# Kernel tuning notes

Hardware: AMD Instinct MI355X
Metric: run time of the kernel (lower is better)

Reference implementation:

```python
import jax, jax.numpy as jnp
import numpy as np

S, B, D, H, DH = 1024, 4, 1024, 16, 64


def setup_inputs() -> dict:
    key = jax.random.key(0)
    ks = jax.random.split(key, 12)
    inp = {
        "query": jax.random.normal(ks[0], (S, B, D), dtype=jnp.float32),
        "key": jax.random.normal(ks[1], (S, B, D), dtype=jnp.float32),
        "value": jax.random.normal(ks[2], (S, B, D), dtype=jnp.float32),
        "key_mask": jax.random.randint(ks[3], (S, B), 0, 2, dtype=jnp.int32),
        # per-head stacked projection weights (original loops nn.Linear per head)
        "Wq": jax.random.normal(ks[4], (H, D, DH), dtype=jnp.float32) * 0.02,
        "bq": jnp.zeros((H, DH), dtype=jnp.float32),
        "Wk": jax.random.normal(ks[5], (H, D, DH), dtype=jnp.float32) * 0.02,
        "bk": jnp.zeros((H, DH), dtype=jnp.float32),
        "Wv": jax.random.normal(ks[6], (H, D, DH), dtype=jnp.float32) * 0.02,
        "bv": jnp.zeros((H, DH), dtype=jnp.float32),
        "Wo": jax.random.normal(ks[7], (H * DH, D), dtype=jnp.float32) * 0.02,
        "bo": jnp.zeros((D,), dtype=jnp.float32),
    }
    return inp


def reference(query, key, value, key_mask, Wq, bq, Wk, bk, Wv, bv, Wo, bo):
    # query/key/value: [S, B, D] (seq-major, matching torch einsum 'imk,jmk->imj')
    q = jnp.einsum('smd,hdk->smhk', query, Wq) + bq  # [Sq, B, H, DH]
    k = jnp.einsum('smd,hdk->smhk', key, Wk) + bk    # [Sk, B, H, DH]
    v = jnp.einsum('smd,hdk->smhk', value, Wv) + bv  # [Sk, B, H, DH]

    scale = 1.0 / jnp.sqrt(jnp.float32(DH))
    scores = jnp.einsum('imhk,jmhk->himj', q, k) * scale  # [H, Sq, B, Sk]
    # key_mask: [Sk, B] -> transpose -> [B, Sk]; additive -1e18 masking
    scores = scores - key_mask.astype(jnp.float32).T * 1e18
    attn = jax.nn.softmax(scores, axis=-1)
    out = jnp.einsum('himj,jmhk->imhk', attn, v)  # [Sq, B, H, DH]
    concat = out.reshape(out.shape[0], out.shape[1], H * DH)
    return concat @ Wo + bo  # [Sq, B, D]
```

## Files before the change

kernel.cpp:

```cpp
#include <hip/hip_runtime.h>
#include <hip/hip_bf16.h>


typedef __attribute__((ext_vector_type(8))) short short8;
typedef __attribute__((ext_vector_type(4))) short short4_;
typedef __attribute__((ext_vector_type(4))) float f32x4;
typedef __attribute__((ext_vector_type(16))) float f32x16;
typedef __attribute__((ext_vector_type(8))) __bf16 bf16x8;
typedef __attribute__((ext_vector_type(4))) __bf16 bf16x4;

union B8 {
    short8 s;
    bf16x8 b;
    unsigned short u[8];
};
union B4 {
    short4_ s;
    bf16x4 b;
    unsigned short u[4];
    int i[2];
};

#if __has_builtin(__builtin_amdgcn_exp2f)
#define EXP2(x) __builtin_amdgcn_exp2f(x)
#else
#define EXP2(x) exp2f(x)
#endif
#if __has_builtin(__builtin_amdgcn_rcpf)
#define RCP(x) __builtin_amdgcn_rcpf(x)
#else
#define RCP(x) (1.0f / (x))
#endif

static __device__ __forceinline__ unsigned short f2bf_rne(float f) {
    union { float f; unsigned u; } v; v.f = f;
    unsigned r = v.u + 0x7FFFu + ((v.u >> 16) & 1u);
    return (unsigned short)(r >> 16);
}

static __device__ __forceinline__ void async_lds16(const void* g, const void* l) {
    __builtin_amdgcn_global_load_lds(
        (const __attribute__((address_space(1))) unsigned int*)(unsigned long long)g,
        (__attribute__((address_space(3))) unsigned int*)(unsigned int)(unsigned long long)l,
        16, 0, 0);
}

__global__ __launch_bounds__(256) void prep(
    const float* __restrict__ Wq, const float* __restrict__ Wk,
    const float* __restrict__ Wv, const float* __restrict__ Wo,
    const float* __restrict__ query, const float* __restrict__ key,
    const float* __restrict__ value,
    unsigned short* __restrict__ WT,
    unsigned short* __restrict__ qA, unsigned short* __restrict__ kA,
    unsigned short* __restrict__ vA) {
    const int t = threadIdx.x;
    const int z = blockIdx.z;

    if (z >= 4) {
        const int zz = z - 4;
        const int tensor = zz >> 2;
        const int part = zz & 3;
        const float* src = (tensor == 0) ? query : (tensor == 1) ? key : value;
        unsigned short* dst = (tensor == 0) ? qA : (tensor == 1) ? kA : vA;
        const int blk = blockIdx.y * 16 + blockIdx.x;
        const size_t base = (size_t)part * 1048576 + (size_t)blk * 4096 + t * 16;
        B8 w0, w1;
#pragma unroll
        for (int i = 0; i < 2; ++i) {
            f32x4 a = *(const f32x4*)(src + base + i * 8);
            f32x4 b = *(const f32x4*)(src + base + i * 8 + 4);
#pragma unroll
            for (int j = 0; j < 4; ++j) {
                (i ? w1 : w0).u[j] = f2bf_rne(a[j]);
                (i ? w1 : w0).u[4 + j] = f2bf_rne(b[j]);
            }
        }
        *(short8*)(dst + base) = w0.s;
        *(short8*)(dst + base + 8) = w1.s;
        return;
    }

    __shared__ float sT[64][65];
    const int dtile = blockIdx.x;
    const int sub = blockIdx.y;
    const float* src;
    int spitch;
    unsigned short* dst;
    if (z < 3) {
        const float* W = (z == 0) ? Wq : (z == 1) ? Wk : Wv;
        src = W + (size_t)sub * 65536 + (size_t)dtile * 64 * 64;
        spitch = 64;
        dst = WT + (size_t)z * 1048576 + (size_t)(sub * 64) * 1024 + dtile * 64;
    } else {
        src = Wo + (size_t)dtile * 64 * 1024 + sub * 64;
        spitch = 1024;
        dst = WT + (size_t)3 * 1048576 + (size_t)(sub * 64) * 1024 + dtile * 64;
    }

    const int r = t >> 2;
    const int cseg = (t & 3) * 16;
#pragma unroll
    for (int i = 0; i < 4; ++i) {
        f32x4 v = *(const f32x4*)(src + (size_t)r * spitch + cseg + i * 4);
#pragma unroll
        for (int j = 0; j < 4; ++j) sT[r][cseg + i * 4 + j] = v[j];
    }
    __syncthreads();
    B8 w0, w1;
#pragma unroll
    for (int i = 0; i < 8; ++i) {
        w0.u[i] = f2bf_rne(sT[cseg + i][r]);
        w1.u[i] = f2bf_rne(sT[cseg + 8 + i][r]);
    }
    *(short8*)(dst + (size_t)r * 1024 + cseg) = w0.s;
    *(short8*)(dst + (size_t)r * 1024 + cseg + 8) = w1.s;
}

template <bool OUT_F32>
__device__ __forceinline__ void gemm128(const unsigned short* __restrict__ A,
                                        const unsigned short* __restrict__ Bt,
                                        const float* __restrict__ bias,
                                        void* __restrict__ Cv, float oscale) {
    __shared__ unsigned short sA[128 * 64];
    __shared__ unsigned short sB[128 * 64];
    const int t = threadIdx.x;
    const int w = t >> 6;
    const int lane = t & 63;
    const int quad = lane >> 4;
    const int l15 = lane & 15;
    const int wr = w >> 1;
    const int wc = w & 1;
    const int row0 = blockIdx.x * 128;
    const int col0 = blockIdx.y * 128;
    const int lrow8 = lane >> 3;
    const int lseg = lane & 7;

    f32x4 acc[4][4] = {};

    for (int k0 = 0; k0 < 1024; k0 += 64) {
#pragma unroll
        for (int i = 0; i < 4; ++i) {
            const int rr = w * 32 + i * 8;
            async_lds16(A + (size_t)(row0 + rr + lrow8) * 1024 + k0 + lseg * 8,
                        &sA[rr * 64]);
            async_lds16(Bt + (size_t)(col0 + rr + lrow8) * 1024 + k0 + lseg * 8,
                        &sB[rr * 64]);
        }
        __syncthreads();
#pragma unroll
        for (int kf = 0; kf < 2; ++kf) {
            B8 af[4], bf[4];
#pragma unroll
            for (int i = 0; i < 4; ++i)
                af[i].s = *(const short8*)&sA[(wr * 64 + i * 16 + l15) * 64 + kf * 32 + quad * 8];
#pragma unroll
            for (int j = 0; j < 4; ++j)
                bf[j].s = *(const short8*)&sB[(wc * 64 + j * 16 + l15) * 64 + kf * 32 + quad * 8];
#pragma unroll
            for (int i = 0; i < 4; ++i)
#pragma unroll
                for (int j = 0; j < 4; ++j)
                    acc[i][j] = __builtin_amdgcn_mfma_f32_16x16x32_bf16(af[i].b, bf[j].b,
                                                                        acc[i][j], 0, 0, 0);
        }
        __syncthreads();
    }
#pragma unroll
    for (int j = 0; j < 4; ++j) {
        const int col = col0 + wc * 64 + j * 16 + l15;
        const float bb = bias[col];
#pragma unroll
        for (int i = 0; i < 4; ++i) {
#pragma unroll
            for (int r = 0; r < 4; ++r) {
                const int row = row0 + wr * 64 + i * 16 + quad * 4 + r;
                const size_t idx = (size_t)row * 1024 + col;
                const float val = (acc[i][j][r] + bb) * oscale;
                if constexpr (OUT_F32)
                    ((float*)Cv)[idx] = val;
                else
                    ((unsigned short*)Cv)[idx] = f2bf_rne(val);
            }
        }
    }
}

#define SCALE_L2E 0.18033688011112042f

__global__ __launch_bounds__(256) void qkv_gemm(
    const unsigned short* __restrict__ qA, const unsigned short* __restrict__ kA,
    const unsigned short* __restrict__ vA,
    const unsigned short* __restrict__ WT,
    const float* __restrict__ bq, const float* __restrict__ bk, const float* __restrict__ bv,
    unsigned short* q_o, unsigned short* k_o, unsigned short* v_o) {
    const int p = blockIdx.z;
    const unsigned short* A = (p == 0) ? qA : (p == 1) ? kA : vA;
    const unsigned short* Bt = WT + (size_t)p * 1048576;
    const float* bias = (p == 0) ? bq : (p == 1) ? bk : bv;
    unsigned short* C = (p == 0) ? q_o : (p == 1) ? k_o : v_o;
    const float osc = (p == 0) ? SCALE_L2E : 1.0f;
    gemm128<false>(A, Bt, bias, C, osc);
}

__global__ __launch_bounds__(256) void out_gemm(const unsigned short* __restrict__ A,
                                                const unsigned short* __restrict__ WT,
                                                const float* __restrict__ bo,
                                                float* __restrict__ C) {
    gemm128<true>(A, WT + (size_t)3 * 1048576, bo, C, 1.0f);
}

#define TP 72

#if __has_builtin(__builtin_amdgcn_mfma_f32_32x32x8bf16_1k)
#define HAVE_X8 1
#endif

__global__ __launch_bounds__(256) void attn_kernel(
    const unsigned short* __restrict__ q,
    const unsigned short* __restrict__ k,
    const unsigned short* __restrict__ v,
    const int* __restrict__ key_mask,
    unsigned short* __restrict__ o) {
    __shared__ unsigned short sK[2][64 * TP];
    __shared__ unsigned short sVt[2][64 * TP];
    __shared__ unsigned long long sBits[16];

    const int t = threadIdx.x;
    const int wave = t >> 6;
    const int lane = t & 63;
    const int n31 = lane & 31;
    const int hh = lane >> 5;

    const int L = blockIdx.x + 8 * (blockIdx.y + 4 * blockIdx.z);
    const int xcd = L & 7;
    const int kk = L >> 3;
    const int g = (xcd << 3) | (kk >> 3);
    const int qt = kk & 7;
    const int b = g & 3;
    const int h = g >> 2;
    const int q0w = qt * 128 + wave * 32;

    const int srow = t >> 3;
    const int sseg = t & 7;

#pragma unroll
    for (int i = 0; i < 4; ++i) {
        const int idx = i * 4 + wave;
        const int sk = idx * 64 + lane;
        unsigned long long bal = __ballot(key_mask[sk * 4 + b] != 0);
        if (lane == 0) sBits[idx] = bal;
    }

    bf16x8 qf[4];
    {
        const unsigned short* qrow =
            q + ((size_t)(q0w + n31) * 4 + b) * 1024 + h * 64 + hh * 8;
#pragma unroll
        for (int kc = 0; kc < 4; ++kc) {
            B8 tmp;
            tmp.s = *(const short8*)(qrow + kc * 16);
            qf[kc] = tmp.b;
        }
    }

    f32x16 O0 = {}, O1 = {}, L_ = {};
    B4 ones;
#pragma unroll
    for (int j = 0; j < 4; ++j) ones.u[j] = 0x3F80;
#if !defined(HAVE_X8)
    B8 ones8;
#pragma unroll
    for (int j = 0; j < 8; ++j) ones8.u[j] = 0x3F80;
#endif

    const unsigned short* kbase = k + (size_t)b * 1024 + h * 64;
    const unsigned short* vbase = v + (size_t)b * 1024 + h * 64;

    {
        const unsigned short* kr = kbase + (size_t)srow * 4096 + sseg * 8;
        short8 ka = *(const short8*)kr;
        short8 kb2 = *(const short8*)(kr + (size_t)32 * 4096);
        const unsigned short* vr = vbase + (size_t)srow * 4096 + sseg * 8;
        B8 va, vb2;
        va.s = *(const short8*)vr;
        vb2.s = *(const short8*)(vr + (size_t)32 * 4096);
        *(short8*)&sK[0][srow * TP + sseg * 8] = ka;
        *(short8*)&sK[0][(32 + srow) * TP + sseg * 8] = kb2;
#pragma unroll
        for (int s = 0; s < 8; ++s) {
            const int j = (s + srow + sseg) & 7;
            sVt[0][(sseg * 8 + j) * TP + srow] = va.u[j];
            sVt[0][(sseg * 8 + j) * TP + 32 + srow] = vb2.u[j];
        }
    }

#pragma unroll 2
    for (int kt = 0; kt < 16; ++kt) {
        const int cur = kt & 1;
        __syncthreads();
        short8 nka, nkb;
        B8 nva, nvb;
        if (kt < 15) {
            const int k0n = (kt + 1) * 64;
            const unsigned short* kr = kbase + (size_t)(k0n + srow) * 4096 + sseg * 8;
            nka = *(const short8*)kr;
            nkb = *(const short8*)(kr + (size_t)32 * 4096);
            const unsigned short* vr = vbase + (size_t)(k0n + srow) * 4096 + sseg * 8;
            nva.s = *(const short8*)vr;
            nvb.s = *(const short8*)(vr + (size_t)32 * 4096);
        }
        const unsigned long long bits = sBits[kt];
        const unsigned long long bsel = bits >> (hh * 4);
        B4 pfr[2][4];
#pragma unroll
        for (int blk = 0; blk < 2; ++blk) {
            const unsigned bw = (unsigned)(bsel >> (blk * 32));
            f32x16 c;
#pragma unroll
            for (int i = 0; i < 4; ++i)
#pragma unroll
                for (int j = 0; j < 4; ++j)
                    c[i * 4 + j] = ((bw >> (j + 8 * i)) & 1u) ? -16384.0f : 0.0f;
            __builtin_amdgcn_s_setprio(1);
#pragma unroll
            for (int kc = 0; kc < 4; ++kc) {
                B8 af;
                af.s = *(const short8*)&sK[cur][(blk * 32 + n31) * TP + kc * 16 + hh * 8];
                c = __builtin_amdgcn_mfma_f32_32x32x16_bf16(af.b, qf[kc], c, 0, 0, 0);
            }
            __builtin_amdgcn_s_setprio(0);
#pragma unroll
            for (int gg = 0; gg < 4; ++gg)
#pragma unroll
                for (int j = 0; j < 4; ++j)
                    pfr[blk][gg].b[j] = (__bf16)EXP2(c[gg * 4 + j]);
        }
#if defined(HAVE_X8)
        __builtin_amdgcn_s_setprio(1);
#pragma unroll
        for (int blk = 0; blk < 2; ++blk) {
#pragma unroll
            for (int gg = 0; gg < 4; ++gg) {
                const int sko = blk * 32 + gg * 8 + hh * 4;
                B4 b0, b1;
                b0.s = *(const short4_*)&sVt[cur][n31 * TP + sko];
                b1.s = *(const short4_*)&sVt[cur][(32 + n31) * TP + sko];
                O0 = __builtin_amdgcn_mfma_f32_32x32x8bf16_1k(pfr[blk][gg].s, b0.s, O0, 0, 0, 0);
                O1 = __builtin_amdgcn_mfma_f32_32x32x8bf16_1k(pfr[blk][gg].s, b1.s, O1, 0, 0, 0);
                L_ = __builtin_amdgcn_mfma_f32_32x32x8bf16_1k(pfr[blk][gg].s, ones.s, L_, 0, 0, 0);
            }
        }
        __builtin_amdgcn_s_setprio(0);
#else
        __builtin_amdgcn_s_setprio(1);
#pragma unroll
        for (int blk = 0; blk < 2; ++blk) {
            B4 par[4];
#pragma unroll
            for (int gg = 0; gg < 4; ++gg) {
                par[gg].i[0] = __shfl_xor(pfr[blk][gg].i[0], 32);
                par[gg].i[1] = __shfl_xor(pfr[blk][gg].i[1], 32);
            }
#pragma unroll
            for (int w = 0; w < 2; ++w) {
                const int gsel = 2 * w + hh;
                B4 lo = (hh == 0) ? pfr[blk][gsel] : par[gsel];
                B4 hi = (hh == 0) ? par[gsel] : pfr[blk][gsel];
                B8 afr;
#pragma unroll
                for (int j = 0; j < 4; ++j) {
                    afr.u[j] = lo.u[j];
                    afr.u[4 + j] = hi.u[j];
                }
                const int sko = blk * 32 + w * 16 + hh * 8;
                B8 b0, b1;
                b0.s = *(const short8*)&sVt[cur][n31 * TP + sko];
                b1.s = *(const short8*)&sVt[cur][(32 + n31) * TP + sko];
                O0 = __builtin_amdgcn_mfma_f32_32x32x16_bf16(afr.b, b0.b, O0, 0, 0, 0);
                O1 = __builtin_amdgcn_mfma_f32_32x32x16_bf16(afr.b, b1.b, O1, 0, 0, 0);
                L_ = __builtin_amdgcn_mfma_f32_32x32x16_bf16(afr.b, ones8.b, L_, 0, 0, 0);
            }
        }
        __builtin_amdgcn_s_setprio(0);
#endif
        if (kt < 15) {
            const int nb = 1 - cur;
            *(short8*)&sK[nb][srow * TP + sseg * 8] = nka;
            *(short8*)&sK[nb][(32 + srow) * TP + sseg * 8] = nkb;
#pragma unroll
            for (int s = 0; s < 8; ++s) {
                const int j = (s + srow + sseg) & 7;
                sVt[nb][(sseg * 8 + j) * TP + srow] = nva.u[j];
                sVt[nb][(sseg * 8 + j) * TP + 32 + srow] = nvb.u[j];
            }
        }
    }

    unsigned short* obase = o + ((size_t)q0w * 4 + b) * 1024 + h * 64 + n31;
#pragma unroll
    for (int r = 0; r < 16; ++r) {
        const int qr = (r & 3) + 8 * (r >> 2) + 4 * hh;
        const float inv = RCP(L_[r]);
        obase[(size_t)qr * 4096] = f2bf_rne(O0[r] * inv);
        obase[(size_t)qr * 4096 + 32] = f2bf_rne(O1[r] * inv);
    }
}

extern "C" void kernel_launch(void* const* d_in, const int* in_sizes, int n_in,
                              void* d_out, int out_size, void* d_ws, size_t ws_size,
                              hipStream_t stream) {
    const float* query = (const float*)d_in[0];
    const float* key_ = (const float*)d_in[1];
    const float* value = (const float*)d_in[2];
    const int* key_mask = (const int*)d_in[3];
    const float* Wq = (const float*)d_in[4];
    const float* bq = (const float*)d_in[5];
    const float* Wk = (const float*)d_in[6];
    const float* bk = (const float*)d_in[7];
    const float* Wv = (const float*)d_in[8];
    const float* bv = (const float*)d_in[9];
    const float* Wo = (const float*)d_in[10];
    const float* bo = (const float*)d_in[11];
    float* out = (float*)d_out;

    const size_t NE = (size_t)4096 * 1024;
    unsigned short* q_ws = (unsigned short*)d_ws;
    unsigned short* k_ws = q_ws + NE;
    unsigned short* v_ws = k_ws + NE;
    unsigned short* a_ws = v_ws + NE;
    unsigned short* wt_ws = a_ws + NE;

    unsigned short* qA = a_ws;
    unsigned short* kA = (unsigned short*)d_out;
    unsigned short* vA = kA + NE;

    prep<<<dim3(16, 16, 16), 256, 0, stream>>>(Wq, Wk, Wv, Wo, query, key_, value,
                                               wt_ws, qA, kA, vA);
    qkv_gemm<<<dim3(32, 8, 3), 256, 0, stream>>>(qA, kA, vA, wt_ws,
                                                 bq, bk, bv, q_ws, k_ws, v_ws);
    attn_kernel<<<dim3(8, 4, 16), 256, 0, stream>>>(q_ws, k_ws, v_ws, key_mask, a_ws);
    out_gemm<<<dim3(32, 8, 1), 256, 0, stream>>>(a_ws, wt_ws, bo, out);
}
```

Before: 243.7 us.

## Emit V pre-transposed from projection GEMM and precompute mask bias in LDS

The V projection is now computed as W_v^T times value per batch, so the GEMM writes V already transposed (head-dim rows, sequence columns) with a row-wise bias. The attention kernel can then fill its transposed-V tile with vector stores instead of sixteen scalar 2-byte LDS writes per thread per tile. The mask-to-bias expansion is also precomputed once into a shared float table and read as vector loads, replacing per-element bit extraction inside the loop. In exchange the V GEMM uses a strided B operand (ldb 4096), the kernel uses 4KB more LDS, and an extra barrier is added.

After: 224.5 us. 7.9% less time.

```diff
diff --git a/kernel.cpp b/kernel.cpp
--- a/kernel.cpp
+++ b/kernel.cpp
@@ -116,11 +116,14 @@
     *(short8*)(dst + (size_t)r * 1024 + cseg + 8) = w1.s;
 }
 
-template <bool OUT_F32>
+template <bool OUT_F32, bool BIAS_ROW>
 __device__ __forceinline__ void gemm128(const unsigned short* __restrict__ A,
+                                        size_t lda,
                                         const unsigned short* __restrict__ Bt,
+                                        size_t ldb,
                                         const float* __restrict__ bias,
-                                        void* __restrict__ Cv, float oscale) {
+                                        void* __restrict__ Cv, size_t ldc,
+                                        float oscale, int row0, int col0) {
     __shared__ unsigned short sA[128 * 64];
     __shared__ unsigned short sB[128 * 64];
     const int t = threadIdx.x;
@@ -130,8 +133,6 @@
     const int l15 = lane & 15;
     const int wr = w >> 1;
     const int wc = w & 1;
-    const int row0 = blockIdx.x * 128;
-    const int col0 = blockIdx.y * 128;
     const int lrow8 = lane >> 3;
     const int lseg = lane & 7;
 
@@ -141,9 +142,9 @@
 #pragma unroll
         for (int i = 0; i < 4; ++i) {
             const int rr = w * 32 + i * 8;
-            async_lds16(A + (size_t)(row0 + rr + lrow8) * 1024 + k0 + lseg * 8,
+            async_lds16(A + (size_t)(row0 + rr + lrow8) * lda + k0 + lseg * 8,
                         &sA[rr * 64]);
-            async_lds16(Bt + (size_t)(col0 + rr + lrow8) * 1024 + k0 + lseg * 8,
+            async_lds16(Bt + (size_t)(col0 + rr + lrow8) * ldb + k0 + lseg * 8,
                         &sB[rr * 64]);
         }
         __syncthreads();
@@ -165,16 +166,25 @@
         }
         __syncthreads();
     }
+    float brow[4][4];
+    if constexpr (BIAS_ROW) {
+#pragma unroll
+        for (int i = 0; i < 4; ++i)
+#pragma unroll
+            for (int r = 0; r < 4; ++r)
+                brow[i][r] = bias[row0 + wr * 64 + i * 16 + quad * 4 + r];
+    }
 #pragma unroll
     for (int j = 0; j < 4; ++j) {
         const int col = col0 + wc * 64 + j * 16 + l15;
-        const float bb = bias[col];
+        const float bcol = BIAS_ROW ? 0.0f : bias[col];
 #pragma unroll
         for (int i = 0; i < 4; ++i) {
 #pragma unroll
             for (int r = 0; r < 4; ++r) {
                 const int row = row0 + wr * 64 + i * 16 + quad * 4 + r;
-                const size_t idx = (size_t)row * 1024 + col;
+                const size_t idx = (size_t)row * ldc + col;
+                const float bb = BIAS_ROW ? brow[i][r] : bcol;
                 const float val = (acc[i][j][r] + bb) * oscale;
                 if constexpr (OUT_F32)
                     ((float*)Cv)[idx] = val;
@@ -192,21 +202,32 @@
     const unsigned short* __restrict__ vA,
     const unsigned short* __restrict__ WT,
     const float* __restrict__ bq, const float* __restrict__ bk, const float* __restrict__ bv,
-    unsigned short* q_o, unsigned short* k_o, unsigned short* v_o) {
+    unsigned short* q_o, unsigned short* k_o, unsigned short* vT_o) {
     const int p = blockIdx.z;
-    const unsigned short* A = (p == 0) ? qA : (p == 1) ? kA : vA;
-    const unsigned short* Bt = WT + (size_t)p * 1048576;
-    const float* bias = (p == 0) ? bq : (p == 1) ? bk : bv;
-    unsigned short* C = (p == 0) ? q_o : (p == 1) ? k_o : v_o;
-    const float osc = (p == 0) ? SCALE_L2E : 1.0f;
-    gemm128<false>(A, Bt, bias, C, osc);
+    if (p < 2) {
+        const unsigned short* A = (p == 0) ? qA : kA;
+        const unsigned short* Bt = WT + (size_t)p * 1048576;
+        const float* bias = (p == 0) ? bq : bk;
+        unsigned short* C = (p == 0) ? q_o : k_o;
+        const float osc = (p == 0) ? SCALE_L2E : 1.0f;
+        gemm128<false, false>(A, 1024, Bt, 1024, bias, C, 1024, osc,
+                              blockIdx.x * 128, blockIdx.y * 128);
+    } else {
+        const int b = blockIdx.x >> 3;
+        const int rt = blockIdx.x & 7;
+        gemm128<false, true>(WT + (size_t)2 * 1048576, 1024,
+                             vA + (size_t)b * 1024, 4096, bv,
+                             vT_o + (size_t)b * 1048576, 1024, 1.0f,
+                             rt * 128, blockIdx.y * 128);
+    }
 }
 
 __global__ __launch_bounds__(256) void out_gemm(const unsigned short* __restrict__ A,
                                                 const unsigned short* __restrict__ WT,
                                                 const float* __restrict__ bo,
                                                 float* __restrict__ C) {
-    gemm128<true>(A, WT + (size_t)3 * 1048576, bo, C, 1.0f);
+    gemm128<true, false>(A, 1024, WT + (size_t)3 * 1048576, 1024, bo, C, 1024, 1.0f,
+                         blockIdx.x * 128, blockIdx.y * 128);
 }
 
 #define TP 72
@@ -218,11 +239,12 @@
 __global__ __launch_bounds__(256) void attn_kernel(
     const unsigned short* __restrict__ q,
     const unsigned short* __restrict__ k,
-    const unsigned short* __restrict__ v,
+    const unsigned short* __restrict__ vT,
     const int* __restrict__ key_mask,
     unsigned short* __restrict__ o) {
     __shared__ unsigned short sK[2][64 * TP];
     __shared__ unsigned short sVt[2][64 * TP];
+    __shared__ float sBias[1024];
     __shared__ unsigned long long sBits[16];
 
     const int t = threadIdx.x;
@@ -250,6 +272,17 @@
         unsigned long long bal = __ballot(key_mask[sk * 4 + b] != 0);
         if (lane == 0) sBits[idx] = bal;
     }
+    __syncthreads();
+#pragma unroll
+    for (int i = 0; i < 4; ++i) {
+        const int idx = t * 4 + i;
+        const int r = idx & 15;
+        const int hb = (idx >> 4) & 1;
+        const int blk = (idx >> 5) & 1;
+        const int kt = idx >> 6;
+        const int row = (r & 3) + 8 * (r >> 2) + 4 * hb + blk * 32;
+        sBias[idx] = ((sBits[kt] >> row) & 1ull) ? -16384.0f : 0.0f;
+    }
 
     bf16x8 qf[4];
     {
@@ -274,53 +307,46 @@
 #endif
 
     const unsigned short* kbase = k + (size_t)b * 1024 + h * 64;
-    const unsigned short* vbase = v + (size_t)b * 1024 + h * 64;
+    const unsigned short* vtb = vT + ((size_t)(b * 16 + h) * 64) * 1024;
 
     {
         const unsigned short* kr = kbase + (size_t)srow * 4096 + sseg * 8;
         short8 ka = *(const short8*)kr;
         short8 kb2 = *(const short8*)(kr + (size_t)32 * 4096);
-        const unsigned short* vr = vbase + (size_t)srow * 4096 + sseg * 8;
-        B8 va, vb2;
-        va.s = *(const short8*)vr;
-        vb2.s = *(const short8*)(vr + (size_t)32 * 4096);
+        const unsigned short* vr = vtb + (size_t)srow * 1024 + sseg * 8;
+        short8 va = *(const short8*)vr;
+        short8 vb2 = *(const short8*)(vr + (size_t)32 * 1024);
         *(short8*)&sK[0][srow * TP + sseg * 8] = ka;
         *(short8*)&sK[0][(32 + srow) * TP + sseg * 8] = kb2;
-#pragma unroll
-        for (int s = 0; s < 8; ++s) {
-            const int j = (s + srow + sseg) & 7;
-            sVt[0][(sseg * 8 + j) * TP + srow] = va.u[j];
-            sVt[0][(sseg * 8 + j) * TP + 32 + srow] = vb2.u[j];
-        }
+        *(short8*)&sVt[0][srow * TP + sseg * 8] = va;
+        *(short8*)&sVt[0][(32 + srow) * TP + sseg * 8] = vb2;
     }
 
 #pragma unroll 2
     for (int kt = 0; kt < 16; ++kt) {
         const int cur = kt & 1;
         __syncthreads();
-        short8 nka, nkb;
-        B8 nva, nvb;
+        short8 nka, nkb, nva, nvb;
         if (kt < 15) {
             const int k0n = (kt + 1) * 64;
             const unsigned short* kr = kbase + (size_t)(k0n + srow) * 4096 + sseg * 8;
             nka = *(const short8*)kr;
             nkb = *(const short8*)(kr + (size_t)32 * 4096);
-            const unsigned short* vr = vbase + (size_t)(k0n + srow) * 4096 + sseg * 8;
-            nva.s = *(const short8*)vr;
-            nvb.s = *(const short8*)(vr + (size_t)32 * 4096);
-        }
-        const unsigned long long bits = sBits[kt];
-        const unsigned long long bsel = bits >> (hh * 4);
+            const unsigned short* vr = vtb + (size_t)srow * 1024 + k0n + sseg * 8;
+            nva = *(const short8*)vr;
+            nvb = *(const short8*)(vr + (size_t)32 * 1024);
+        }
         B4 pfr[2][4];
 #pragma unroll
         for (int blk = 0; blk < 2; ++blk) {
-            const unsigned bw = (unsigned)(bsel >> (blk * 32));
             f32x16 c;
-#pragma unroll
-            for (int i = 0; i < 4; ++i)
-#pragma unroll
-                for (int j = 0; j < 4; ++j)
-                    c[i * 4 + j] = ((bw >> (j + 8 * i)) & 1u) ? -16384.0f : 0.0f;
+            const f32x4* bp = (const f32x4*)&sBias[((kt * 2 + blk) * 2 + hh) * 16];
+#pragma unroll
+            for (int i = 0; i < 4; ++i) {
+                f32x4 x = bp[i];
+#pragma unroll
+                for (int j = 0; j < 4; ++j) c[i * 4 + j] = x[j];
+            }
             __builtin_amdgcn_s_setprio(1);
 #pragma unroll
             for (int kc = 0; kc < 4; ++kc) {
@@ -387,12 +413,8 @@
             const int nb = 1 - cur;
             *(short8*)&sK[nb][srow * TP + sseg * 8] = nka;
             *(short8*)&sK[nb][(32 + srow) * TP + sseg * 8] = nkb;
-#pragma unroll
-            for (int s = 0; s < 8; ++s) {
-                const int j = (s + srow + sseg) & 7;
-                sVt[nb][(sseg * 8 + j) * TP + srow] = nva.u[j];
-                sVt[nb][(sseg * 8 + j) * TP + 32 + srow] = nvb.u[j];
-            }
+            *(short8*)&sVt[nb][srow * TP + sseg * 8] = nva;
+            *(short8*)&sVt[nb][(32 + srow) * TP + sseg * 8] = nvb;
         }
     }
 
```
